# Performance work log

Measured on AMD Instinct MI355X. Metric: run time of the kernel, lower is better.

## Reference

```python
import jax, jax.numpy as jnp
import numpy as np

N_USERS = 100000
N_MOVIES = 20000
D = 64
R = 5
E = 400000


def setup_inputs() -> dict:
    key = jax.random.key(0)
    ks = jax.random.split(key, 20)
    s = 0.1  # xavier-ish scale
    return {
        'edges_u': jax.random.randint(ks[0], (R, E), 0, N_USERS, dtype=jnp.int32),
        'edges_m': jax.random.randint(ks[1], (R, E), 0, N_MOVIES, dtype=jnp.int32),
        'review_feat': jax.random.normal(ks[2], (R, E, D), jnp.float32),
        'W_user': jax.random.normal(ks[3], (R, N_USERS, D), jnp.float32) * s,
        'W_movie': jax.random.normal(ks[4], (R, N_MOVIES, D), jnp.float32) * s,
        'ps_u': jax.random.normal(ks[5], (R, D), jnp.float32) * s,
        'rs_u': jax.random.normal(ks[6], (R, D), jnp.float32) * s,
        'rw_u': jax.random.normal(ks[7], (R, D, D), jnp.float32) * s,
        'ps_m': jax.random.normal(ks[8], (R, D), jnp.float32) * s,
        'rs_m': jax.random.normal(ks[9], (R, D), jnp.float32) * s,
        'rw_m': jax.random.normal(ks[10], (R, D, D), jnp.float32) * s,
        'user_cj': jax.random.uniform(ks[11], (N_USERS, 1), jnp.float32),
        'user_ci': jax.random.uniform(ks[12], (N_USERS, 1), jnp.float32),
        'movie_cj': jax.random.uniform(ks[13], (N_MOVIES, 1), jnp.float32),
        'movie_ci': jax.random.uniform(ks[14], (N_MOVIES, 1), jnp.float32),
        'ufc_w': jax.random.normal(ks[15], (D, D), jnp.float32) * s,
        'ufc_b': jax.random.normal(ks[16], (D,), jnp.float32) * s,
        'ifc_w': jax.random.normal(ks[17], (D, D), jnp.float32) * s,
        'ifc_b': jax.random.normal(ks[18], (D,), jnp.float32) * s,
    }


def _conv_one_rel(h_src, rfeat, ps, rs, rw, cj_src, e_src, e_dst, n_dst):
    # h_src: [Nsrc, D] (the GCMC 'weight'-as-embedding), rfeat: [E, D]
    pa = jax.nn.sigmoid(rfeat @ ps)[:, None]                       # [E,1]
    rf = (rfeat @ rw.T) * jax.nn.sigmoid(rfeat @ rs)[:, None]      # [E,D]
    m = (h_src[e_src] * pa + rf) * cj_src[e_src]                   # gather->elemwise
    return jax.ops.segment_sum(m, e_dst, num_segments=n_dst)       # scatter-sum [Ndst,D]


def reference(edges_u, edges_m, review_feat, W_user, W_movie,
              ps_u, rs_u, rw_u, ps_m, rs_m, rw_m,
              user_cj, user_ci, movie_cj, movie_ci,
              ufc_w, ufc_b, ifc_w, ifc_b):
    # forward etypes (user -> movie), per rating, summed by HeteroGraphConv
    movie_agg = jax.vmap(
        lambda h, rf_, p, r_, w, eu, em: _conv_one_rel(h, rf_, p, r_, w, user_cj, eu, em, N_MOVIES)
    )(W_user, review_feat, ps_u, rs_u, rw_u, edges_u, edges_m).sum(0)
    # reverse etypes (movie -> user)
    user_agg = jax.vmap(
        lambda h, rf_, p, r_, w, em, eu: _conv_one_rel(h, rf_, p, r_, w, movie_cj, em, eu, N_USERS)
    )(W_movie, review_feat, ps_m, rs_m, rw_m, edges_m, edges_u).sum(0)

    ufeat = user_agg * user_ci    # dst normalization
    ifeat = movie_agg * movie_ci
    ufeat = jax.nn.gelu(ufeat, approximate=False)
    ifeat = jax.nn.gelu(ifeat, approximate=False)
    ufeat = ufeat @ ufc_w.T + ufc_b
    ifeat = ifeat @ ifc_w.T + ifc_b
    return ufeat, ifeat
```

## Files before the change

kernel.cpp:

```cpp
#include <hip/hip_runtime.h>
#include <hip/hip_bf16.h>

#define NU 100000
#define NM 20000
#define DD 64
#define RR 5
#define EE 400000
#define NE (RR * EE)
#define NNODE (NM + NU)
#define NTILE (EE / 16)
#define NCHUNK ((NNODE + 1023) / 1024)
#define GM_BLOCKS (NM / 4)
#define GU_BLOCKS (NU / 32)

typedef __attribute__((ext_vector_type(8))) short bf16x8;
typedef __attribute__((ext_vector_type(8))) short s16x8;
typedef __attribute__((ext_vector_type(4))) int   i32x4;
typedef __attribute__((ext_vector_type(4))) float f32x4;

static __device__ __forceinline__ short f2bf(float f) {
  return __builtin_bit_cast(short, __float2bfloat16(f));
}
static __device__ __forceinline__ float bf2f(short s) {
  return __builtin_bit_cast(float, ((unsigned)(unsigned short)s) << 16);
}

static __device__ __forceinline__ f32x4 ntl_f4(const float* __restrict__ p) {
  return __builtin_nontemporal_load((const f32x4*)p);
}

static __device__ __forceinline__ bf16x8 pack8e(const f32x4 a, const f32x4 b) {
  bf16x8 o;
  o[0] = f2bf(a.x); o[1] = f2bf(a.y); o[2] = f2bf(a.z); o[3] = f2bf(a.w);
  o[4] = f2bf(b.x); o[5] = f2bf(b.y); o[6] = f2bf(b.z); o[7] = f2bf(b.w);
  return o;
}
static __device__ __forceinline__ bf16x8 cvt8(const float* __restrict__ p) {
  return pack8e(*(const f32x4*)p, *(const f32x4*)(p + 4));
}

static __device__ __forceinline__ float sigm(float x) { return 1.f / (1.f + __expf(-x)); }
static __device__ __forceinline__ float gelu(float x) {
  return 0.5f * x * (1.f + erff(x * 0.70710678118654752f));
}

__global__ __launch_bounds__(256) void rank0_k(const int* __restrict__ eu,
                                               const int* __restrict__ em,
                                               int* __restrict__ cnt,
                                               int* __restrict__ rank_m,
                                               int* __restrict__ rank_u) {
  const int i = (blockIdx.x * 256 + threadIdx.x) * 4;
  if (i < NE) {
    const i32x4 a = *(const i32x4*)(em + i);
    const i32x4 b = *(const i32x4*)(eu + i);
    i32x4 rm, ru;
    rm.x = atomicAdd(&cnt[a.x], 1);
    rm.y = atomicAdd(&cnt[a.y], 1);
    rm.z = atomicAdd(&cnt[a.z], 1);
    rm.w = atomicAdd(&cnt[a.w], 1);
    ru.x = atomicAdd(&cnt[NM + b.x], 1);
    ru.y = atomicAdd(&cnt[NM + b.y], 1);
    ru.z = atomicAdd(&cnt[NM + b.z], 1);
    ru.w = atomicAdd(&cnt[NM + b.w], 1);
    *(i32x4*)(rank_m + i) = rm;
    *(i32x4*)(rank_u + i) = ru;
  }
}

__global__ __launch_bounds__(256) void scan_k(const int* __restrict__ cnt,
                                              int* __restrict__ cursor,
                                              int* __restrict__ off) {
  const int b = blockIdx.x;
  const int t = threadIdx.x;
  const int idx = b * 1024 + t * 4;
  i32x4 v = {0, 0, 0, 0};
  if (idx + 3 < NNODE) v = *(const i32x4*)(cnt + idx);
  else {
    if (idx     < NNODE) v.x = cnt[idx];
    if (idx + 1 < NNODE) v.y = cnt[idx + 1];
    if (idx + 2 < NNODE) v.z = cnt[idx + 2];
    if (idx + 3 < NNODE) v.w = cnt[idx + 3];
  }
  const int s = v.x + v.y + v.z + v.w;
  __shared__ int sh[256];
  __shared__ int base_sh;
  sh[t] = s;
  __syncthreads();
  for (int d = 1; d < 256; d <<= 1) {
    const int x = (t >= d) ? sh[t - d] : 0;
    __syncthreads();
    sh[t] += x;
    __syncthreads();
  }
  if (t == 255) base_sh = atomicAdd(cursor, sh[255]);
  __syncthreads();
  const int pre = base_sh + sh[t] - s;
  i32x4 o;
  o.x = pre;
  o.y = pre + v.x;
  o.z = pre + v.x + v.y;
  o.w = pre + v.x + v.y + v.z;
  if (idx + 3 < NNODE) *(i32x4*)(off + idx) = o;
  else {
    if (idx     < NNODE) off[idx]     = o.x;
    if (idx + 1 < NNODE) off[idx + 1] = o.y;
    if (idx + 2 < NNODE) off[idx + 2] = o.z;
    if (idx + 3 < NNODE) off[idx + 3] = o.w;
  }
}

__global__ __launch_bounds__(256) void gcmc_main(
    const int* __restrict__ edges_u, const int* __restrict__ edges_m,
    const float* __restrict__ rfeat,
    const float* __restrict__ W_user, const float* __restrict__ W_movie,
    const float* __restrict__ ps_u, const float* __restrict__ rs_u, const float* __restrict__ rw_u,
    const float* __restrict__ ps_m, const float* __restrict__ rs_m, const float* __restrict__ rw_m,
    const float* __restrict__ user_cj, const float* __restrict__ movie_cj,
    const int* __restrict__ rank_m, const int* __restrict__ rank_u,
    const int* __restrict__ off,
    short* __restrict__ msg)
{
  const int r    = blockIdx.y;
  const int lane = threadIdx.x & 63;
  const int wid  = threadIdx.x >> 6;
  const int c    = lane & 15;
  const int kr   = lane >> 4;
  const int wtile = blockIdx.x * 4 + wid;
  if (wtile >= NTILE / 8) return;

  bf16x8 Bu[4][2], Bm[4][2], Bs[2];
#pragma unroll
  for (int t = 0; t < 4; ++t) {
#pragma unroll
    for (int s = 0; s < 2; ++s) {
      Bu[t][s] = cvt8(rw_u + ((size_t)r * DD + (4 * c + t)) * DD + s * 32 + kr * 8);
      Bm[t][s] = cvt8(rw_m + ((size_t)r * DD + (4 * c + t)) * DD + s * 32 + kr * 8);
    }
  }
#pragma unroll
  for (int s = 0; s < 2; ++s) {
    if (c < 4) {
      const float* v = (c == 0 ? rs_u : c == 1 ? ps_u : c == 2 ? rs_m : ps_m)
                       + r * DD + s * 32 + kr * 8;
      Bs[s] = cvt8(v);
    } else {
      bf16x8 z = {0, 0, 0, 0, 0, 0, 0, 0};
      Bs[s] = z;
    }
  }

#pragma unroll 1
  for (int tt = 0; tt < 8; ++tt) {
    const int tile = wtile * 8 + tt;
    const int e0 = tile * 16;

    const float* arow = rfeat + ((size_t)r * EE + e0 + c) * DD + kr * 8;
    const f32x4 fa0 = ntl_f4(arow);
    const f32x4 fa1 = ntl_f4(arow + 4);
    const f32x4 fa2 = ntl_f4(arow + 32);
    const f32x4 fa3 = ntl_f4(arow + 36);

    const int ebase = r * EE + e0 + kr * 4;
    const i32x4 eu4  = *(const i32x4*)(edges_u + ebase);
    const i32x4 em4  = *(const i32x4*)(edges_m + ebase);
    const i32x4 rm4  = *(const i32x4*)(rank_m + ebase);
    const i32x4 ru4  = *(const i32x4*)(rank_u + ebase);
    const int eus[4] = {eu4.x, eu4.y, eu4.z, eu4.w};
    const int ems[4] = {em4.x, em4.y, em4.z, em4.w};
    const int rms[4] = {rm4.x, rm4.y, rm4.z, rm4.w};
    const int rus[4] = {ru4.x, ru4.y, ru4.z, ru4.w};

    int slm[4], slu[4];
    float cju[4], cjm[4];
    f32x4 hu[4], hm[4];
#pragma unroll
    for (int q = 0; q < 4; ++q) {
      slm[q] = off[ems[q]] + rms[q];
      slu[q] = off[NM + eus[q]] + rus[q];
      cju[q] = user_cj[eus[q]];
      cjm[q] = movie_cj[ems[q]];
      hu[q]  = *(const f32x4*)(W_user  + ((size_t)r * NU + eus[q]) * DD + 4 * c);
      hm[q]  = *(const f32x4*)(W_movie + ((size_t)r * NM + ems[q]) * DD + 4 * c);
    }

    const bf16x8 A0 = pack8e(fa0, fa1);
    const bf16x8 A1 = pack8e(fa2, fa3);
    f32x4 z4 = {0.f, 0.f, 0.f, 0.f};
    f32x4 Cu[4], Cm[4], Cs;
#pragma unroll
    for (int t = 0; t < 4; ++t) { Cu[t] = z4; Cm[t] = z4; }
    Cs = z4;
#pragma unroll
    for (int t = 0; t < 4; ++t) {
      Cu[t] = __builtin_amdgcn_mfma_f32_16x16x32_bf16(A0, Bu[t][0], Cu[t], 0, 0, 0);
      Cu[t] = __builtin_amdgcn_mfma_f32_16x16x32_bf16(A1, Bu[t][1], Cu[t], 0, 0, 0);
      Cm[t] = __builtin_amdgcn_mfma_f32_16x16x32_bf16(A0, Bm[t][0], Cm[t], 0, 0, 0);
      Cm[t] = __builtin_amdgcn_mfma_f32_16x16x32_bf16(A1, Bm[t][1], Cm[t], 0, 0, 0);
    }
    Cs = __builtin_amdgcn_mfma_f32_16x16x32_bf16(A0, Bs[0], Cs, 0, 0, 0);
    Cs = __builtin_amdgcn_mfma_f32_16x16x32_bf16(A1, Bs[1], Cs, 0, 0, 0);

#pragma unroll
    for (int q = 0; q < 4; ++q) {
      const int src = (lane & 48);
      const float su = __shfl(Cs[q], src);
      const float pu = __shfl(Cs[q], src | 1);
      const float sm = __shfl(Cs[q], src | 2);
      const float pm = __shfl(Cs[q], src | 3);
      const float sgu = sigm(su), pau = sigm(pu);
      const float sgm_ = sigm(sm), pam = sigm(pm);

      short4 vm, vu;
      vm.x = f2bf((hu[q].x * pau + Cu[0][q] * sgu) * cju[q]);
      vm.y = f2bf((hu[q].y * pau + Cu[1][q] * sgu) * cju[q]);
      vm.z = f2bf((hu[q].z * pau + Cu[2][q] * sgu) * cju[q]);
      vm.w = f2bf((hu[q].w * pau + Cu[3][q] * sgu) * cju[q]);
      vu.x = f2bf((hm[q].x * pam + Cm[0][q] * sgm_) * cjm[q]);
      vu.y = f2bf((hm[q].y * pam + Cm[1][q] * sgm_) * cjm[q]);
      vu.z = f2bf((hm[q].z * pam + Cm[2][q] * sgm_) * cjm[q]);
      vu.w = f2bf((hm[q].w * pam + Cm[3][q] * sgm_) * cjm[q]);

      *(short4*)(msg + ((size_t)slm[q] << 6) + 4 * c) = vm;
      *(short4*)(msg + ((size_t)slu[q] << 6) + 4 * c) = vu;
    }
  }
}

__global__ __launch_bounds__(256) void gather_k(const int* __restrict__ off,
                                                const int* __restrict__ cnt,
                                                const short* __restrict__ msg,
                                                float* __restrict__ out)
{
  if (blockIdx.x < GM_BLOCKS) {
    const int w    = blockIdx.x * 4 + (threadIdx.x >> 6);
    const int lane = threadIdx.x & 63;
    const int sub  = lane >> 3;
    const int c8   = lane & 7;

    const int s0 = off[w];
    const int e1 = s0 + cnt[w];

    float a0[8] = {0,0,0,0,0,0,0,0};
    float a1[8] = {0,0,0,0,0,0,0,0};
    float a2[8] = {0,0,0,0,0,0,0,0};
    float a3[8] = {0,0,0,0,0,0,0,0};
    int k = s0 + sub;
    for (; k + 24 < e1; k += 32) {
      const s16x8 v0 = *(const s16x8*)(msg + ((size_t)k << 6) + 8 * c8);
      const s16x8 v1 = *(const s16x8*)(msg + ((size_t)(k + 8) << 6) + 8 * c8);
      const s16x8 v2 = *(const s16x8*)(msg + ((size_t)(k + 16) << 6) + 8 * c8);
      const s16x8 v3 = *(const s16x8*)(msg + ((size_t)(k + 24) << 6) + 8 * c8);
#pragma unroll
      for (int j = 0; j < 8; ++j) {
        a0[j] += bf2f(v0[j]); a1[j] += bf2f(v1[j]);
        a2[j] += bf2f(v2[j]); a3[j] += bf2f(v3[j]);
      }
    }
    for (; k < e1; k += 8) {
      const s16x8 v0 = *(const s16x8*)(msg + ((size_t)k << 6) + 8 * c8);
#pragma unroll
      for (int j = 0; j < 8; ++j) a0[j] += bf2f(v0[j]);
    }
#pragma unroll
    for (int j = 0; j < 8; ++j) {
      a0[j] += a1[j] + a2[j] + a3[j];
      a0[j] += __shfl_xor(a0[j], 8);
      a0[j] += __shfl_xor(a0[j], 16);
      a0[j] += __shfl_xor(a0[j], 32);
    }
    if (sub == 0) {
      float* dst = out + (size_t)NU * DD + (size_t)w * DD + 8 * c8;
      f32x4 o0 = {a0[0], a0[1], a0[2], a0[3]};
      f32x4 o1 = {a0[4], a0[5], a0[6], a0[7]};
      *(f32x4*)dst = o0;
      *(f32x4*)(dst + 4) = o1;
    }
  } else {
    const int u  = (blockIdx.x - GM_BLOCKS) * 32 + (threadIdx.x >> 3);
    const int c8 = threadIdx.x & 7;

    const int s0 = off[NM + u];
    const int e1 = s0 + cnt[NM + u];

    float a0[8] = {0,0,0,0,0,0,0,0};
    float a1[8] = {0,0,0,0,0,0,0,0};
    float a2[8] = {0,0,0,0,0,0,0,0};
    float a3[8] = {0,0,0,0,0,0,0,0};
    int k = s0;
    for (; k + 3 < e1; k += 4) {
      const s16x8 v0 = *(const s16x8*)(msg + ((size_t)k << 6) + 8 * c8);
      const s16x8 v1 = *(const s16x8*)(msg + ((size_t)(k + 1) << 6) + 8 * c8);
      const s16x8 v2 = *(const s16x8*)(msg + ((size_t)(k + 2) << 6) + 8 * c8);
      const s16x8 v3 = *(const s16x8*)(msg + ((size_t)(k + 3) << 6) + 8 * c8);
#pragma unroll
      for (int j = 0; j < 8; ++j) {
        a0[j] += bf2f(v0[j]); a1[j] += bf2f(v1[j]);
        a2[j] += bf2f(v2[j]); a3[j] += bf2f(v3[j]);
      }
    }
    for (; k < e1; ++k) {
      const s16x8 v0 = *(const s16x8*)(msg + ((size_t)k << 6) + 8 * c8);
#pragma unroll
      for (int j = 0; j < 8; ++j) a0[j] += bf2f(v0[j]);
    }
    float* dst = out + (size_t)u * DD + 8 * c8;
    f32x4 o0, o1;
    o0.x = a0[0] + a1[0] + a2[0] + a3[0];
    o0.y = a0[1] + a1[1] + a2[1] + a3[1];
    o0.z = a0[2] + a1[2] + a2[2] + a3[2];
    o0.w = a0[3] + a1[3] + a2[3] + a3[3];
    o1.x = a0[4] + a1[4] + a2[4] + a3[4];
    o1.y = a0[5] + a1[5] + a2[5] + a3[5];
    o1.z = a0[6] + a1[6] + a2[6] + a3[6];
    o1.w = a0[7] + a1[7] + a2[7] + a3[7];
    *(f32x4*)dst = o0;
    *(f32x4*)(dst + 4) = o1;
  }
}

__global__ __launch_bounds__(256) void gcmc_fc(
    float* __restrict__ out,
    const float* __restrict__ user_ci, const float* __restrict__ movie_ci,
    const float* __restrict__ ufc_w, const float* __restrict__ ufc_b,
    const float* __restrict__ ifc_w, const float* __restrict__ ifc_b)
{
  const int wt   = blockIdx.x * 4 + (threadIdx.x >> 6);
  const int lane = threadIdx.x & 63;
  const int c    = lane & 15;
  const int kr   = lane >> 4;
  const bool isU = wt < (NU / 16);
  float* base        = isU ? out : out + (size_t)NU * DD;
  const float* ci    = isU ? user_ci : movie_ci;
  const float* W     = isU ? ufc_w : ifc_w;
  const float* bias  = isU ? ufc_b : ifc_b;
  const int row0 = (isU ? wt : wt - (NU / 16)) * 16;

  bf16x8 B[4][2];
#pragma unroll
  for (int t = 0; t < 4; ++t)
#pragma unroll
    for (int s = 0; s < 2; ++s)
      B[t][s] = cvt8(W + (size_t)(4 * c + t) * DD + s * 32 + kr * 8);

  const float civ = ci[row0 + c];
  const float* arow = base + (size_t)(row0 + c) * DD + kr * 8;

  bf16x8 A0, A1;
  {
    const f32x4 a = *(const f32x4*)arow;
    const f32x4 b = *(const f32x4*)(arow + 4);
    const f32x4 a2 = *(const f32x4*)(arow + 32);
    const f32x4 b2 = *(const f32x4*)(arow + 36);
    A0[0] = f2bf(gelu(a.x * civ));  A0[1] = f2bf(gelu(a.y * civ));
    A0[2] = f2bf(gelu(a.z * civ));  A0[3] = f2bf(gelu(a.w * civ));
    A0[4] = f2bf(gelu(b.x * civ));  A0[5] = f2bf(gelu(b.y * civ));
    A0[6] = f2bf(gelu(b.z * civ));  A0[7] = f2bf(gelu(b.w * civ));
    A1[0] = f2bf(gelu(a2.x * civ)); A1[1] = f2bf(gelu(a2.y * civ));
    A1[2] = f2bf(gelu(a2.z * civ)); A1[3] = f2bf(gelu(a2.w * civ));
    A1[4] = f2bf(gelu(b2.x * civ)); A1[5] = f2bf(gelu(b2.y * civ));
    A1[6] = f2bf(gelu(b2.z * civ)); A1[7] = f2bf(gelu(b2.w * civ));
  }

  f32x4 z4 = {0.f, 0.f, 0.f, 0.f};
  f32x4 C[4];
#pragma unroll
  for (int t = 0; t < 4; ++t) {
    C[t] = z4;
    C[t] = __builtin_amdgcn_mfma_f32_16x16x32_bf16(A0, B[t][0], C[t], 0, 0, 0);
    C[t] = __builtin_amdgcn_mfma_f32_16x16x32_bf16(A1, B[t][1], C[t], 0, 0, 0);
  }

  const f32x4 b4 = *(const f32x4*)(bias + 4 * c);
#pragma unroll
  for (int q = 0; q < 4; ++q) {
    const int row = row0 + kr * 4 + q;
    f32x4 o;
    o.x = C[0][q] + b4.x; o.y = C[1][q] + b4.y;
    o.z = C[2][q] + b4.z; o.w = C[3][q] + b4.w;
    *(f32x4*)(base + (size_t)row * DD + 4 * c) = o;
  }
}

extern "C" void kernel_launch(void* const* d_in, const int* in_sizes, int n_in,
                              void* d_out, int out_size, void* d_ws, size_t ws_size,
                              hipStream_t stream) {
  const int*   edges_u  = (const int*)  d_in[0];
  const int*   edges_m  = (const int*)  d_in[1];
  const float* rfeat    = (const float*)d_in[2];
  const float* W_user   = (const float*)d_in[3];
  const float* W_movie  = (const float*)d_in[4];
  const float* ps_u     = (const float*)d_in[5];
  const float* rs_u     = (const float*)d_in[6];
  const float* rw_u     = (const float*)d_in[7];
  const float* ps_m     = (const float*)d_in[8];
  const float* rs_m     = (const float*)d_in[9];
  const float* rw_m     = (const float*)d_in[10];
  const float* user_cj  = (const float*)d_in[11];
  const float* user_ci  = (const float*)d_in[12];
  const float* movie_cj = (const float*)d_in[13];
  const float* movie_ci = (const float*)d_in[14];
  const float* ufc_w    = (const float*)d_in[15];
  const float* ufc_b    = (const float*)d_in[16];
  const float* ifc_w    = (const float*)d_in[17];
  const float* ifc_b    = (const float*)d_in[18];

  float* out = (float*)d_out;

  char* ws = (char*)d_ws;
  size_t o = 0;
  auto alloc = [&](size_t bytes) { char* p = ws + o; o += (bytes + 255) & ~(size_t)255; return p; };
  int*   cnt    = (int*)  alloc(sizeof(int) * NNODE);
  int*   off    = (int*)  alloc(sizeof(int) * NNODE);
  int*   cursor = (int*)  alloc(sizeof(int) * 1);
  int*   rank_m = (int*)  alloc(sizeof(int) * NE);
  int*   rank_u = (int*)  alloc(sizeof(int) * NE);
  short* msg    = (short*)alloc(sizeof(short) * (size_t)2 * NE * DD);
  (void)ws_size;

  hipMemsetAsync(cnt, 0, sizeof(int) * NNODE, stream);
  hipMemsetAsync(cursor, 0, sizeof(int), stream);
  rank0_k<<<(NE / 4 + 255) / 256, 256, 0, stream>>>(edges_u, edges_m, cnt, rank_m, rank_u);
  scan_k<<<NCHUNK, 256, 0, stream>>>(cnt, cursor, off);

  dim3 g1((NTILE / 8 + 3) / 4, RR);
  gcmc_main<<<g1, 256, 0, stream>>>(edges_u, edges_m, rfeat, W_user, W_movie,
                                    ps_u, rs_u, rw_u, ps_m, rs_m, rw_m,
                                    user_cj, movie_cj, rank_m, rank_u, off, msg);

  gather_k<<<GM_BLOCKS + GU_BLOCKS, 256, 0, stream>>>(off, cnt, msg, out);

  gcmc_fc<<<(NNODE / 16) / 4, 256, 0, stream>>>(out, user_ci, movie_ci,
                                                ufc_w, ufc_b, ifc_w, ifc_b);
}
```

Measured before the change: 711.7 us.

## Fuse segment gather with GELU and FC epilogue through shared memory

Merges the gather/segment-sum kernel with the dst-normalization, GELU and MFMA FC kernel. Aggregated rows are staged in LDS per block and one or two wavefronts run the 16-row FC tile, so the intermediate fp32 aggregate no longer takes a global write and read and one launch is dropped. Movie blocks now process 4 movies per wave serially, and only some waves do the FC while the rest idle at the barrier.

Result: faster. 697.1 us (-2.1%).

```diff
diff --git a/kernel.cpp b/kernel.cpp
--- a/kernel.cpp
+++ b/kernel.cpp
@@ -10,8 +10,8 @@
 #define NNODE (NM + NU)
 #define NTILE (EE / 16)
 #define NCHUNK ((NNODE + 1023) / 1024)
-#define GM_BLOCKS (NM / 4)
-#define GU_BLOCKS (NU / 32)
+#define MFB (NM / 16)
+#define UFB (NU / 32)
 
 typedef __attribute__((ext_vector_type(8))) short bf16x8;
 typedef __attribute__((ext_vector_type(8))) short s16x8;
@@ -226,58 +226,114 @@
   }
 }
 
-__global__ __launch_bounds__(256) void gather_k(const int* __restrict__ off,
-                                                const int* __restrict__ cnt,
-                                                const short* __restrict__ msg,
-                                                float* __restrict__ out)
+static __device__ __forceinline__ void fc_tile16(
+    const float (*rows)[68], const float* __restrict__ ci,
+    const float* __restrict__ W, const float* __restrict__ bias,
+    float* __restrict__ dst, const int lane)
 {
-  if (blockIdx.x < GM_BLOCKS) {
-    const int w    = blockIdx.x * 4 + (threadIdx.x >> 6);
-    const int lane = threadIdx.x & 63;
+  const int c  = lane & 15;
+  const int kr = lane >> 4;
+
+  bf16x8 B[4][2];
+#pragma unroll
+  for (int t = 0; t < 4; ++t)
+#pragma unroll
+    for (int s = 0; s < 2; ++s)
+      B[t][s] = cvt8(W + (size_t)(4 * c + t) * DD + s * 32 + kr * 8);
+
+  const float civ = ci[c];
+  bf16x8 A0, A1;
+#pragma unroll
+  for (int j = 0; j < 8; ++j) {
+    A0[j] = f2bf(gelu(rows[c][kr * 8 + j] * civ));
+    A1[j] = f2bf(gelu(rows[c][32 + kr * 8 + j] * civ));
+  }
+
+  f32x4 z4 = {0.f, 0.f, 0.f, 0.f};
+  f32x4 C[4];
+#pragma unroll
+  for (int t = 0; t < 4; ++t) {
+    C[t] = z4;
+    C[t] = __builtin_amdgcn_mfma_f32_16x16x32_bf16(A0, B[t][0], C[t], 0, 0, 0);
+    C[t] = __builtin_amdgcn_mfma_f32_16x16x32_bf16(A1, B[t][1], C[t], 0, 0, 0);
+  }
+
+  const f32x4 b4 = *(const f32x4*)(bias + 4 * c);
+#pragma unroll
+  for (int q = 0; q < 4; ++q) {
+    f32x4 o;
+    o.x = C[0][q] + b4.x; o.y = C[1][q] + b4.y;
+    o.z = C[2][q] + b4.z; o.w = C[3][q] + b4.w;
+    *(f32x4*)(dst + (size_t)(kr * 4 + q) * DD + 4 * c) = o;
+  }
+}
+
+__global__ __launch_bounds__(256) void gather_fc_k(
+    const int* __restrict__ off, const int* __restrict__ cnt,
+    const short* __restrict__ msg,
+    const float* __restrict__ user_ci, const float* __restrict__ movie_ci,
+    const float* __restrict__ ufc_w, const float* __restrict__ ufc_b,
+    const float* __restrict__ ifc_w, const float* __restrict__ ifc_b,
+    float* __restrict__ out)
+{
+  __shared__ float rows[32][68];
+  const int wid  = threadIdx.x >> 6;
+  const int lane = threadIdx.x & 63;
+
+  if (blockIdx.x < MFB) {
+    const int mblk = blockIdx.x;
     const int sub  = lane >> 3;
     const int c8   = lane & 7;
 
-    const int s0 = off[w];
-    const int e1 = s0 + cnt[w];
-
-    float a0[8] = {0,0,0,0,0,0,0,0};
-    float a1[8] = {0,0,0,0,0,0,0,0};
-    float a2[8] = {0,0,0,0,0,0,0,0};
-    float a3[8] = {0,0,0,0,0,0,0,0};
-    int k = s0 + sub;
-    for (; k + 24 < e1; k += 32) {
-      const s16x8 v0 = *(const s16x8*)(msg + ((size_t)k << 6) + 8 * c8);
-      const s16x8 v1 = *(const s16x8*)(msg + ((size_t)(k + 8) << 6) + 8 * c8);
-      const s16x8 v2 = *(const s16x8*)(msg + ((size_t)(k + 16) << 6) + 8 * c8);
-      const s16x8 v3 = *(const s16x8*)(msg + ((size_t)(k + 24) << 6) + 8 * c8);
+#pragma unroll 1
+    for (int mm = 0; mm < 4; ++mm) {
+      const int mlocal = wid * 4 + mm;
+      const int w = mblk * 16 + mlocal;
+      const int s0 = off[w];
+      const int e1 = s0 + cnt[w];
+
+      float a0[8] = {0,0,0,0,0,0,0,0};
+      float a1[8] = {0,0,0,0,0,0,0,0};
+      float a2[8] = {0,0,0,0,0,0,0,0};
+      float a3[8] = {0,0,0,0,0,0,0,0};
+      int k = s0 + sub;
+      for (; k + 24 < e1; k += 32) {
+        const s16x8 v0 = *(const s16x8*)(msg + ((size_t)k << 6) + 8 * c8);
+        const s16x8 v1 = *(const s16x8*)(msg + ((size_t)(k + 8) << 6) + 8 * c8);
+        const s16x8 v2 = *(const s16x8*)(msg + ((size_t)(k + 16) << 6) + 8 * c8);
+        const s16x8 v3 = *(const s16x8*)(msg + ((size_t)(k + 24) << 6) + 8 * c8);
+#pragma unroll
+        for (int j = 0; j < 8; ++j) {
+          a0[j] += bf2f(v0[j]); a1[j] += bf2f(v1[j]);
+          a2[j] += bf2f(v2[j]); a3[j] += bf2f(v3[j]);
+        }
+      }
+      for (; k < e1; k += 8) {
+        const s16x8 v0 = *(const s16x8*)(msg + ((size_t)k << 6) + 8 * c8);
+#pragma unroll
+        for (int j = 0; j < 8; ++j) a0[j] += bf2f(v0[j]);
+      }
 #pragma unroll
       for (int j = 0; j < 8; ++j) {
-        a0[j] += bf2f(v0[j]); a1[j] += bf2f(v1[j]);
-        a2[j] += bf2f(v2[j]); a3[j] += bf2f(v3[j]);
+        a0[j] += a1[j] + a2[j] + a3[j];
+        a0[j] += __shfl_xor(a0[j], 8);
+        a0[j] += __shfl_xor(a0[j], 16);
+        a0[j] += __shfl_xor(a0[j], 32);
       }
-    }
-    for (; k < e1; k += 8) {
-      const s16x8 v0 = *(const s16x8*)(msg + ((size_t)k << 6) + 8 * c8);
-#pragma unroll
-      for (int j = 0; j < 8; ++j) a0[j] += bf2f(v0[j]);
-    }
-#pragma unroll
-    for (int j = 0; j < 8; ++j) {
-      a0[j] += a1[j] + a2[j] + a3[j];
-      a0[j] += __shfl_xor(a0[j], 8);
-      a0[j] += __shfl_xor(a0[j], 16);
-      a0[j] += __shfl_xor(a0[j], 32);
-    }
-    if (sub == 0) {
-      float* dst = out + (size_t)NU * DD + (size_t)w * DD + 8 * c8;
-      f32x4 o0 = {a0[0], a0[1], a0[2], a0[3]};
-      f32x4 o1 = {a0[4], a0[5], a0[6], a0[7]};
-      *(f32x4*)dst = o0;
-      *(f32x4*)(dst + 4) = o1;
-    }
+      if (sub == 0) {
+#pragma unroll
+        for (int j = 0; j < 8; ++j) rows[mlocal][8 * c8 + j] = a0[j];
+      }
+    }
+    __syncthreads();
+    if (wid == 0)
+      fc_tile16(rows, movie_ci + mblk * 16, ifc_w, ifc_b,
+                out + (size_t)NU * DD + (size_t)mblk * 16 * DD, lane);
   } else {
-    const int u  = (blockIdx.x - GM_BLOCKS) * 32 + (threadIdx.x >> 3);
-    const int c8 = threadIdx.x & 7;
+    const int ublk = blockIdx.x - MFB;
+    const int ul   = threadIdx.x >> 3;
+    const int c8   = threadIdx.x & 7;
+    const int u    = ublk * 32 + ul;
 
     const int s0 = off[NM + u];
     const int e1 = s0 + cnt[NM + u];
@@ -303,81 +359,13 @@
 #pragma unroll
       for (int j = 0; j < 8; ++j) a0[j] += bf2f(v0[j]);
     }
-    float* dst = out + (size_t)u * DD + 8 * c8;
-    f32x4 o0, o1;
-    o0.x = a0[0] + a1[0] + a2[0] + a3[0];
-    o0.y = a0[1] + a1[1] + a2[1] + a3[1];
-    o0.z = a0[2] + a1[2] + a2[2] + a3[2];
-    o0.w = a0[3] + a1[3] + a2[3] + a3[3];
-    o1.x = a0[4] + a1[4] + a2[4] + a3[4];
-    o1.y = a0[5] + a1[5] + a2[5] + a3[5];
-    o1.z = a0[6] + a1[6] + a2[6] + a3[6];
-    o1.w = a0[7] + a1[7] + a2[7] + a3[7];
-    *(f32x4*)dst = o0;
-    *(f32x4*)(dst + 4) = o1;
-  }
-}
-
-__global__ __launch_bounds__(256) void gcmc_fc(
-    float* __restrict__ out,
-    const float* __restrict__ user_ci, const float* __restrict__ movie_ci,
-    const float* __restrict__ ufc_w, const float* __restrict__ ufc_b,
-    const float* __restrict__ ifc_w, const float* __restrict__ ifc_b)
-{
-  const int wt   = blockIdx.x * 4 + (threadIdx.x >> 6);
-  const int lane = threadIdx.x & 63;
-  const int c    = lane & 15;
-  const int kr   = lane >> 4;
-  const bool isU = wt < (NU / 16);
-  float* base        = isU ? out : out + (size_t)NU * DD;
-  const float* ci    = isU ? user_ci : movie_ci;
-  const float* W     = isU ? ufc_w : ifc_w;
-  const float* bias  = isU ? ufc_b : ifc_b;
-  const int row0 = (isU ? wt : wt - (NU / 16)) * 16;
-
-  bf16x8 B[4][2];
-#pragma unroll
-  for (int t = 0; t < 4; ++t)
-#pragma unroll
-    for (int s = 0; s < 2; ++s)
-      B[t][s] = cvt8(W + (size_t)(4 * c + t) * DD + s * 32 + kr * 8);
-
-  const float civ = ci[row0 + c];
-  const float* arow = base + (size_t)(row0 + c) * DD + kr * 8;
-
-  bf16x8 A0, A1;
-  {
-    const f32x4 a = *(const f32x4*)arow;
-    const f32x4 b = *(const f32x4*)(arow + 4);
-    const f32x4 a2 = *(const f32x4*)(arow + 32);
-    const f32x4 b2 = *(const f32x4*)(arow + 36);
-    A0[0] = f2bf(gelu(a.x * civ));  A0[1] = f2bf(gelu(a.y * civ));
-    A0[2] = f2bf(gelu(a.z * civ));  A0[3] = f2bf(gelu(a.w * civ));
-    A0[4] = f2bf(gelu(b.x * civ));  A0[5] = f2bf(gelu(b.y * civ));
-    A0[6] = f2bf(gelu(b.z * civ));  A0[7] = f2bf(gelu(b.w * civ));
-    A1[0] = f2bf(gelu(a2.x * civ)); A1[1] = f2bf(gelu(a2.y * civ));
-    A1[2] = f2bf(gelu(a2.z * civ)); A1[3] = f2bf(gelu(a2.w * civ));
-    A1[4] = f2bf(gelu(b2.x * civ)); A1[5] = f2bf(gelu(b2.y * civ));
-    A1[6] = f2bf(gelu(b2.z * civ)); A1[7] = f2bf(gelu(b2.w * civ));
-  }
-
-  f32x4 z4 = {0.f, 0.f, 0.f, 0.f};
-  f32x4 C[4];
-#pragma unroll
-  for (int t = 0; t < 4; ++t) {
-    C[t] = z4;
-    C[t] = __builtin_amdgcn_mfma_f32_16x16x32_bf16(A0, B[t][0], C[t], 0, 0, 0);
-    C[t] = __builtin_amdgcn_mfma_f32_16x16x32_bf16(A1, B[t][1], C[t], 0, 0, 0);
-  }
-
-  const f32x4 b4 = *(const f32x4*)(bias + 4 * c);
-#pragma unroll
-  for (int q = 0; q < 4; ++q) {
-    const int row = row0 + kr * 4 + q;
-    f32x4 o;
-    o.x = C[0][q] + b4.x; o.y = C[1][q] + b4.y;
-    o.z = C[2][q] + b4.z; o.w = C[3][q] + b4.w;
-    *(f32x4*)(base + (size_t)row * DD + 4 * c) = o;
+#pragma unroll
+    for (int j = 0; j < 8; ++j) rows[ul][8 * c8 + j] = a0[j] + a1[j] + a2[j] + a3[j];
+
+    __syncthreads();
+    if (wid < 2)
+      fc_tile16(rows + wid * 16, user_ci + ublk * 32 + wid * 16, ufc_w, ufc_b,
+                out + (size_t)(ublk * 32 + wid * 16) * DD, lane);
   }
 }
 
@@ -427,8 +415,7 @@
                                     ps_u, rs_u, rw_u, ps_m, rs_m, rw_m,
                                     user_cj, movie_cj, rank_m, rank_u, off, msg);
 
-  gather_k<<<GM_BLOCKS + GU_BLOCKS, 256, 0, stream>>>(off, cnt, msg, out);
-
-  gcmc_fc<<<(NNODE / 16) / 4, 256, 0, stream>>>(out, user_ci, movie_ci,
-                                                ufc_w, ufc_b, ifc_w, ifc_b);
-}
+  gather_fc_k<<<MFB + UFB, 256, 0, stream>>>(off, cnt, msg,
+                                             user_ci, movie_ci,
+                                             ufc_w, ufc_b, ifc_w, ifc_b, out);
+}
```
